# Optimization experiments

Measured on AMD Instinct MI355X. Metric: run time of the kernel, lower is better.

## Reference

```python
import jax, jax.numpy as jnp
import numpy as np

# Module hyperparameters (mirror init_kwargs)
SI = 32   # size_in
K = 3     # size_kern
IC = 16   # in_channels
OC = 32   # out_channels
SO = SI - K + 1  # size_out = 30
B = 32
NUM_COLS = OC * SO * SO


def build_indices():
    """Replicates generate_sparse_weights for connect_type='regular'.
    row = (i+k1)*SI + (j+k2) + k*SI^2, col = y*SO^2 + i*SO + j,
    vidx = (y*IC + k)*K^2 + k1*K + k2."""
    y = np.arange(OC)[:, None, None, None, None, None]
    i = np.arange(SO)[None, :, None, None, None, None]
    j = np.arange(SO)[None, None, :, None, None, None]
    k = np.arange(IC)[None, None, None, :, None, None]
    k1 = np.arange(K)[None, None, None, None, :, None]
    k2 = np.arange(K)[None, None, None, None, None, :]
    shape = (OC, SO, SO, IC, K, K)
    rows = np.broadcast_to((i + k1) * SI + (j + k2) + k * SI * SI, shape).ravel().astype(np.int32)
    cols = np.broadcast_to(y * SO * SO + i * SO + j, shape).ravel().astype(np.int32)
    vidx = np.broadcast_to((y * IC + k) * K * K + k1 * K + k2, shape).ravel().astype(np.int32)
    return rows, cols, vidx


def setup_inputs() -> dict:
    key = jax.random.key(0)
    kx, kw = jax.random.split(key)
    x = jax.random.normal(kx, (B, IC, SI, SI), dtype=jnp.float32)
    # flat conv weight, like nn.Conv2d(IC, OC, K).weight.reshape(-1)
    fan_in = IC * K * K
    bound = 1.0 / np.sqrt(fan_in)
    weight = jax.random.uniform(kw, (OC * IC * K * K,), dtype=jnp.float32,
                                minval=-bound, maxval=bound)
    bias = jnp.zeros((OC,), dtype=jnp.float32)
    rows, cols, vidx = build_indices()
    return {"x": x, "weight": weight, "bias": bias,
            "rows": jnp.asarray(rows), "cols": jnp.asarray(cols),
            "param_idx": jnp.asarray(vidx)}


def reference(x, weight, bias, rows, cols, param_idx):
    # gather weight values per nnz entry, gather input rows, scatter-add to output cols
    wv = weight[param_idx]                       # [nnz]
    xf = x.reshape(x.shape[0], IC * SI * SI)     # [B, IC*SI^2]
    contrib = xf[:, rows] * wv[None, :]          # [B, nnz]
    out = jax.ops.segment_sum(contrib.T, cols, num_segments=NUM_COLS).T  # [B, OC*SO^2]
    out = out.reshape(-1, OC, SO, SO)
    out = out + bias[:, None, None]
    return out
```

## Files before the change

### kernel.cpp

```cpp
#include <hip/hip_runtime.h>

#define BATCH 32
#define IC 16
#define OC 32
#define SI 32
#define KS 3
#define SO 30

#define ROWS 4
#define XROWS (ROWS + KS - 1)
#define XCOLS 36
#define NBANDS 8
#define RTOT (IC * KS * KS)

__global__ __launch_bounds__(512) void conv3x3_kernel(
    const float* __restrict__ x, const float* __restrict__ w,
    const float* __restrict__ bias, float* __restrict__ out)
{
    __shared__ __align__(16) float ws[RTOT][OC];
    __shared__ __align__(16) float xs[IC][XROWS][XCOLS];

    const int t    = threadIdx.x;
    const int blk  = blockIdx.x;
    const int band = blk & (NBANDS - 1);
    const int b    = blk >> 3;
    const int row0 = band * ROWS;

    for (int idx = t; idx < RTOT * OC; idx += 512) {
        const int oc = idx & (OC - 1);
        const int r  = idx >> 5;
        ((float*)ws)[idx] = w[oc * RTOT + r];
    }

    const float* xb = x + b * (IC * SI * SI);
    for (int idx = t; idx < IC * XROWS * XCOLS; idx += 512) {
        const int ic  = idx / (XROWS * XCOLS);
        const int rem = idx - ic * (XROWS * XCOLS);
        const int ii  = rem / XCOLS;
        const int jj  = rem - ii * XCOLS;
        const int gi  = row0 + ii;
        float v = 0.0f;
        if (gi < SI && jj < SI) v = xb[ic * SI * SI + gi * SI + jj];
        ((float*)xs)[idx] = v;
    }
    __syncthreads();

    const int duo = t >> 5;
    const int oc0 = duo * 2;
    const int tp  = t & 31;
    const int il  = tp >> 3;
    const int c   = (tp & 7) * 4;

    float acc[2][4] = {{0.f}};

    #pragma unroll 2
    for (int ic = 0; ic < IC; ++ic) {
        #pragma unroll
        for (int k1 = 0; k1 < KS; ++k1) {
            const float4 xa = *reinterpret_cast<const float4*>(&xs[ic][il + k1][c]);
            const float4 xc = *reinterpret_cast<const float4*>(&xs[ic][il + k1][c + 4]);
            const float xw[8] = {xa.x, xa.y, xa.z, xa.w, xc.x, xc.y, xc.z, xc.w};
            #pragma unroll
            for (int k2 = 0; k2 < KS; ++k2) {
                const float2 w2 =
                    *reinterpret_cast<const float2*>(&ws[ic * 9 + k1 * 3 + k2][oc0]);
                #pragma unroll
                for (int jj = 0; jj < 4; ++jj) {
                    acc[0][jj] = fmaf(w2.x, xw[k2 + jj], acc[0][jj]);
                    acc[1][jj] = fmaf(w2.y, xw[k2 + jj], acc[1][jj]);
                }
            }
        }
    }

    const int i = row0 + il;
    if (i < SO) {
        #pragma unroll
        for (int oo = 0; oo < 2; ++oo) {
            const int oc = oc0 + oo;
            const float bs = bias[oc];
            float* orow = out + ((size_t)(b * OC + oc) * SO + i) * SO;
            *reinterpret_cast<float2*>(&orow[c]) =
                make_float2(acc[oo][0] + bs, acc[oo][1] + bs);
            if (c + 3 < SO) {
                *reinterpret_cast<float2*>(&orow[c + 2]) =
                    make_float2(acc[oo][2] + bs, acc[oo][3] + bs);
            }
        }
    }
}

extern "C" void kernel_launch(void* const* d_in, const int* in_sizes, int n_in,
                              void* d_out, int out_size, void* d_ws, size_t ws_size,
                              hipStream_t stream) {
    const float* x    = (const float*)d_in[0];
    const float* w    = (const float*)d_in[1];
    const float* bias = (const float*)d_in[2];
    float* out = (float*)d_out;

    conv3x3_kernel<<<dim3(BATCH * NBANDS), dim3(512), 0, stream>>>(x, w, bias, out);
}
```

Before: 103.2 us.

## Split output channels across two blocks and read weights as wave-uniform scalars

```diff
diff --git a/kernel.cpp b/kernel.cpp
--- a/kernel.cpp
+++ b/kernel.cpp
@@ -11,29 +11,23 @@
 #define XROWS (ROWS + KS - 1)
 #define XCOLS 36
 #define NBANDS 8
-#define RTOT (IC * KS * KS)
+#define WPT (IC * KS * KS)
 
-__global__ __launch_bounds__(512) void conv3x3_kernel(
+__global__ __launch_bounds__(256) void conv3x3_kernel(
     const float* __restrict__ x, const float* __restrict__ w,
     const float* __restrict__ bias, float* __restrict__ out)
 {
-    __shared__ __align__(16) float ws[RTOT][OC];
     __shared__ __align__(16) float xs[IC][XROWS][XCOLS];
 
     const int t    = threadIdx.x;
     const int blk  = blockIdx.x;
     const int band = blk & (NBANDS - 1);
-    const int b    = blk >> 3;
+    const int g    = (blk >> 3) & 1;
+    const int b    = blk >> 4;
     const int row0 = band * ROWS;
 
-    for (int idx = t; idx < RTOT * OC; idx += 512) {
-        const int oc = idx & (OC - 1);
-        const int r  = idx >> 5;
-        ((float*)ws)[idx] = w[oc * RTOT + r];
-    }
-
     const float* xb = x + b * (IC * SI * SI);
-    for (int idx = t; idx < IC * XROWS * XCOLS; idx += 512) {
+    for (int idx = t; idx < IC * XROWS * XCOLS; idx += 256) {
         const int ic  = idx / (XROWS * XCOLS);
         const int rem = idx - ic * (XROWS * XCOLS);
         const int ii  = rem / XCOLS;
@@ -45,47 +39,44 @@
     }
     __syncthreads();
 
-    const int duo = t >> 5;
-    const int oc0 = duo * 2;
-    const int tp  = t & 31;
-    const int il  = tp >> 3;
-    const int c   = (tp & 7) * 4;
+    const int wvid = __builtin_amdgcn_readfirstlane(t >> 6);
+    const int oc0  = g * 16 + wvid * 4;
+    const float* __restrict__ wq = w + oc0 * WPT;
 
-    float acc[2][4] = {{0.f}};
+    const int l  = t & 63;
+    const int il = l >> 4;
+    const int c  = (l & 15) * 2;
+
+    float acc[4][2] = {{0.f}};
 
     #pragma unroll 2
     for (int ic = 0; ic < IC; ++ic) {
         #pragma unroll
         for (int k1 = 0; k1 < KS; ++k1) {
-            const float4 xa = *reinterpret_cast<const float4*>(&xs[ic][il + k1][c]);
-            const float4 xc = *reinterpret_cast<const float4*>(&xs[ic][il + k1][c + 4]);
-            const float xw[8] = {xa.x, xa.y, xa.z, xa.w, xc.x, xc.y, xc.z, xc.w};
+            const float2 xa = *reinterpret_cast<const float2*>(&xs[ic][il + k1][c]);
+            const float2 xc = *reinterpret_cast<const float2*>(&xs[ic][il + k1][c + 2]);
+            const float xw[4] = {xa.x, xa.y, xc.x, xc.y};
             #pragma unroll
             for (int k2 = 0; k2 < KS; ++k2) {
-                const float2 w2 =
-                    *reinterpret_cast<const float2*>(&ws[ic * 9 + k1 * 3 + k2][oc0]);
                 #pragma unroll
-                for (int jj = 0; jj < 4; ++jj) {
-                    acc[0][jj] = fmaf(w2.x, xw[k2 + jj], acc[0][jj]);
-                    acc[1][jj] = fmaf(w2.y, xw[k2 + jj], acc[1][jj]);
+                for (int oo = 0; oo < 4; ++oo) {
+                    const float wv = wq[oo * WPT + ic * 9 + k1 * 3 + k2];
+                    acc[oo][0] = fmaf(wv, xw[k2],     acc[oo][0]);
+                    acc[oo][1] = fmaf(wv, xw[k2 + 1], acc[oo][1]);
                 }
             }
         }
     }
 
     const int i = row0 + il;
-    if (i < SO) {
+    if (i < SO && c < SO) {
         #pragma unroll
-        for (int oo = 0; oo < 2; ++oo) {
+        for (int oo = 0; oo < 4; ++oo) {
             const int oc = oc0 + oo;
             const float bs = bias[oc];
             float* orow = out + ((size_t)(b * OC + oc) * SO + i) * SO;
             *reinterpret_cast<float2*>(&orow[c]) =
                 make_float2(acc[oo][0] + bs, acc[oo][1] + bs);
-            if (c + 3 < SO) {
-                *reinterpret_cast<float2*>(&orow[c + 2]) =
-                    make_float2(acc[oo][2] + bs, acc[oo][3] + bs);
-            }
         }
     }
 }
@@ -98,5 +89,5 @@
     const float* bias = (const float*)d_in[2];
     float* out = (float*)d_out;
 
-    conv3x3_kernel<<<dim3(BATCH * NBANDS), dim3(512), 0, stream>>>(x, w, bias, out);
+    conv3x3_kernel<<<dim3(BATCH * 2 * NBANDS), dim3(256), 0, stream>>>(x, w, bias, out);
 }
```

Result: faster. 97.53 us (-5.5%).
